# Kernel tuning notes

Measured on AMD Instinct MI355X. Metric: run time of the kernel, lower is better.

## Reference

```python
import jax, jax.numpy as jnp
import numpy as np

A_NUM = 9
C_NUM = 20


def generate_anchor(anc, grid):
    # anc: (A,2) w,h ; grid: (B,H,W,2) centers -> anchors (B,A,H,W,4)
    centers = grid[:, None]                      # (B,1,H,W,2)
    half = anc.reshape(1, -1, 1, 1, 2) * 0.5     # (1,A,1,1,2)
    return jnp.concatenate([centers - half, centers + half], axis=-1)


def iou_matrix(proposals, bboxes):
    # proposals: (B,A,H,W,4) -> (B,K,4); bboxes: (B,N,5)
    B = proposals.shape[0]
    p = proposals.reshape(B, -1, 4)[:, :, None, :]   # (B,K,1,4)
    bb = bboxes[:, None, :, :]                       # (B,1,N,5)
    s_p = (p[..., 2] - p[..., 0]) * (p[..., 3] - p[..., 1])
    s_b = (bb[..., 2] - bb[..., 0]) * (bb[..., 3] - bb[..., 1])
    ix1 = jnp.maximum(p[..., 0], bb[..., 0])
    iy1 = jnp.maximum(p[..., 1], bb[..., 1])
    ix2 = jnp.minimum(p[..., 2], bb[..., 2])
    iy2 = jnp.minimum(p[..., 3], bb[..., 3])
    s_i = jnp.clip(ix2 - ix1, 0.0) * jnp.clip(iy2 - iy1, 0.0)
    s_u = s_p + s_b - s_i
    iou = jnp.clip(s_i / (s_u + 1e-8), 0.0)
    invalid = (s_u <= 0) | (s_p <= 0) | (s_b <= 0) | (bb[..., 0] < 0)
    return jnp.where(invalid, 0.0, iou)              # (B,K,N)


def extract_anchor_data(anchor_data, idx):
    # anchor_data: (B,A,D,H,W) -> flat (B*A*H*W, D) -> gather
    B, A, D, H, W = anchor_data.shape
    flat = jnp.transpose(anchor_data, (0, 1, 3, 4, 2)).reshape(-1, D)
    return flat[idx]


def extract_class_scores(all_scores, idx, num_anchors):
    # all_scores: (B,C,H,W) -> (B,A,H,W,C) flat -> gather
    B, C, H, W = all_scores.shape
    s = jnp.transpose(all_scores, (0, 2, 3, 1))[:, None]          # (B,1,H,W,C)
    s = jnp.broadcast_to(s, (B, num_anchors, H, W, C)).reshape(-1, C)
    return s[idx]


def setup_inputs() -> dict:
    key = jax.random.key(0)
    ks = jax.random.split(key, 8)
    B, Cin, H, W = 32, 1280, 28, 28
    N, M = 64, 4096
    hid, out_ch = 128, 5 * A_NUM + C_NUM
    features = jax.random.normal(ks[0], (B, Cin, H, W), dtype=jnp.float32)
    # grid of feature-cell centers (GenerateGrid-style)
    xs = jnp.arange(W, dtype=jnp.float32) + 0.5
    ys = jnp.arange(H, dtype=jnp.float32) + 0.5
    gx, gy = jnp.meshgrid(xs, ys, indexing='xy')
    grid = jnp.broadcast_to(jnp.stack([gx, gy], axis=-1), (B, H, W, 2))
    anc = jnp.array([[1.0, 1], [2, 2], [3, 3], [4, 4], [5, 5], [2, 3], [3, 2], [3, 5], [5, 3]], dtype=jnp.float32)
    tl = jax.random.uniform(ks[1], (B, N, 2), minval=0.0, maxval=20.0)
    wh = jax.random.uniform(ks[2], (B, N, 2), minval=1.0, maxval=8.0)
    cls = jax.random.randint(ks[3], (B, N, 1), 0, C_NUM).astype(jnp.float32)
    bb = jnp.concatenate([tl, tl + wh, cls], axis=-1)
    valid = jax.random.uniform(ks[4], (B, N, 1)) > 0.25
    bboxes = jnp.where(valid, bb, -1.0)
    K = B * A_NUM * H * W
    pos_anchor_idx = jax.random.randint(ks[5], (M,), 0, K, dtype=jnp.int64 if jax.config.jax_enable_x64 else jnp.int32)
    neg_anchor_idx = jax.random.randint(ks[6], (M,), 0, K, dtype=pos_anchor_idx.dtype)
    W1 = jax.random.normal(ks[7], (hid, Cin), dtype=jnp.float32) * 0.02
    b1 = jnp.zeros((hid,), dtype=jnp.float32)
    W2 = jax.random.normal(jax.random.fold_in(key, 99), (out_ch, hid), dtype=jnp.float32) * 0.02
    b2 = jnp.zeros((out_ch,), dtype=jnp.float32)
    return {"features": features, "grid": grid, "anc": anc, "bboxes": bboxes,
            "pos_anchor_idx": pos_anchor_idx, "neg_anchor_idx": neg_anchor_idx,
            "W1": W1, "b1": b1, "W2": W2, "b2": b2}


def reference(features, grid, anc, bboxes, pos_anchor_idx, neg_anchor_idx, W1, b1, W2, b2):
    B, Cin, H, W = features.shape
    A, C = A_NUM, C_NUM
    # anchors + broadcast IoU matrix
    anchors = generate_anchor(anc, grid)                 # (B,A,H,W,4)
    iou_mat = iou_matrix(anchors, bboxes)                # (B,A*H*W,N)
    # prediction head: 1x1 conv -> (dropout eval: identity) -> leaky_relu -> 1x1 conv
    h = jnp.einsum('bchw,oc->bohw', features, W1) + b1[None, :, None, None]
    h = jax.nn.leaky_relu(h, negative_slope=0.01)
    out = jnp.einsum('bchw,oc->bohw', h, W2) + b2[None, :, None, None]  # (B,5A+C,H,W)
    anchor_raw = out[:, :5 * A].reshape(B, A, 5, H, W)
    conf_sq = jax.nn.sigmoid(anchor_raw[:, :, 0:1])      # (B,A,1,H,W)
    off_raw = anchor_raw[:, :, 1:]                       # (B,A,4,H,W)
    off_sq = jnp.concatenate([jax.nn.sigmoid(off_raw[:, :, :2]) - 0.5, off_raw[:, :, 2:]], axis=2)
    class_raw = out[:, 5 * A:]                           # (B,C,H,W)
    # training path: irregular gathers
    class_scores = extract_class_scores(class_raw, pos_anchor_idx, A)   # (M,C)
    offsets = extract_anchor_data(off_sq, pos_anchor_idx)               # (M,4)
    conf_pos = extract_anchor_data(conf_sq, pos_anchor_idx)             # (M,1)
    conf_neg = extract_anchor_data(conf_sq, neg_anchor_idx)             # (M,1)
    conf_scores = jnp.concatenate([conf_pos, conf_neg], axis=0)         # (2M,1)
    return conf_scores, offsets, class_scores, iou_mat
```

## Files before the change

### kernel.cpp

```cpp
#include <hip/hip_runtime.h>
#include <cstdint>

#define A_NUM 9
#define C_NUM 20
#define B_SZ 32
#define HW 784
#define P_NUM (A_NUM*HW)
#define NBOX 64
#define CIN 1280
#define HID 128
#define M_IDX 4096
#define KSPLIT 4
#define KS_PER 10
#define ASTR 40
#define PSTR ((size_t)B_SZ * HW * HID)
#define IOU_PB 64

#define CONF_OFF 0
#define OFFS_OFF (2*M_IDX)
#define CLS_OFF  (OFFS_OFF + 4*M_IDX)
#define IOU_OFF  (CLS_OFF + C_NUM*M_IDX)

typedef short bf16x8 __attribute__((ext_vector_type(8)));
typedef float f32x4  __attribute__((ext_vector_type(4)));

__device__ __forceinline__ unsigned pack_bf16(float lo, float hi) {
  unsigned a = __builtin_bit_cast(unsigned, lo);
  unsigned b = __builtin_bit_cast(unsigned, hi);
  return ((a + 0x8000u) >> 16) | ((b + 0x8000u) & 0xffff0000u);
}

__global__ __launch_bounds__(256) void prep_w1(const float* __restrict__ W1,
                                               uint4* __restrict__ W1f) {
  int id = blockIdx.x * 256 + threadIdx.x;
  int lane = id & 63;
  int ntile = (id >> 6) & 7;
  int ks = id >> 9;
  int lo = lane & 15, quad = lane >> 4;
  int n = ntile * 16 + lo;
  int k0 = ks * 32 + quad * 8;
  const float* src = W1 + n * CIN + k0;
  float4 x = *(const float4*)src;
  float4 y = *(const float4*)(src + 4);
  uint4 p;
  p.x = pack_bf16(x.x, x.y);
  p.y = pack_bf16(x.z, x.w);
  p.z = pack_bf16(y.x, y.y);
  p.w = pack_bf16(y.z, y.w);
  W1f[id] = p;
}

__global__ __launch_bounds__(256) void gemm1_mfma(
    const float* __restrict__ F, const unsigned short* __restrict__ W1f,
    float* __restrict__ Part) {
  __shared__ unsigned short Asm[2][64 * ASTR];

  const int b = blockIdx.y;
  const int z = blockIdx.z;
  const int m0 = blockIdx.x * 64;
  const int t = threadIdx.x;
  const int wave = t >> 6, lane = t & 63;
  const int quad = lane >> 4, lo = lane & 15;
  const int ksbase = z * KS_PER;

  const int sm = t & 63;
  const int kh = t >> 6;
  const int gm = m0 + sm;
  const bool mval = gm < HW;
  const float* Fb = F + (size_t)b * CIN * HW + (mval ? gm : 0);

  f32x4 acc[4][2];
#pragma unroll
  for (int i = 0; i < 4; i++)
#pragma unroll
    for (int j = 0; j < 2; j++) acc[i][j] = (f32x4){0.f, 0.f, 0.f, 0.f};

  float va[8];
  uint4 vb[2][2];

  auto loadA = [&](int kk) {
    const int k0 = (ksbase + kk) * 32 + kh * 8;
#pragma unroll
    for (int i = 0; i < 8; i++) va[i] = Fb[(size_t)(k0 + i) * HW];
  };
  auto loadB = [&](int kk, uint4* dst) {
    const unsigned short* g =
        W1f + (size_t)(((ksbase + kk) * 8 + wave * 2) * 64 + lane) * 8;
    dst[0] = *(const uint4*)g;
    dst[1] = *(const uint4*)(g + 512);
  };
  auto stageA = [&](int buf) {
    uint4 p;
    if (mval) {
      p.x = pack_bf16(va[0], va[1]);
      p.y = pack_bf16(va[2], va[3]);
      p.z = pack_bf16(va[4], va[5]);
      p.w = pack_bf16(va[6], va[7]);
    } else {
      p = (uint4){0, 0, 0, 0};
    }
    *(uint4*)&Asm[buf][sm * ASTR + kh * 8] = p;
  };
  auto compute = [&](int buf, uint4* bv) {
    const unsigned short* Ab = &Asm[buf][lo * ASTR + quad * 8];
    bf16x8 af[4];
#pragma unroll
    for (int i = 0; i < 4; i++) af[i] = *(const bf16x8*)(Ab + i * 16 * ASTR);
    bf16x8 b0 = __builtin_bit_cast(bf16x8, bv[0]);
    bf16x8 b1 = __builtin_bit_cast(bf16x8, bv[1]);
#pragma unroll
    for (int i = 0; i < 4; i++) {
      acc[i][0] = __builtin_amdgcn_mfma_f32_16x16x32_bf16(af[i], b0, acc[i][0], 0, 0, 0);
      acc[i][1] = __builtin_amdgcn_mfma_f32_16x16x32_bf16(af[i], b1, acc[i][1], 0, 0, 0);
    }
  };

  loadA(0);
  loadB(0, vb[0]);
  stageA(0);
  __syncthreads();
  for (int kk = 0; kk < KS_PER; kk++) {
    const int cur = kk & 1;
    if (kk + 1 < KS_PER) {
      loadA(kk + 1);
      loadB(kk + 1, vb[cur ^ 1]);
    }
    compute(cur, vb[cur]);
    if (kk + 1 < KS_PER) stageA(cur ^ 1);
    __syncthreads();
  }

  float* Pz = Part + ((size_t)(z * B_SZ + b) * HW) * HID;
#pragma unroll
  for (int i = 0; i < 4; i++) {
    const int mbase = m0 + i * 16 + quad * 4;
#pragma unroll
    for (int j = 0; j < 2; j++) {
      const int n = wave * 32 + j * 16 + lo;
#pragma unroll
      for (int r = 0; r < 4; r++) {
        const int mm = mbase + r;
        if (mm < HW) Pz[(size_t)mm * HID + n] = acc[i][j][r];
      }
    }
  }
}

__global__ __launch_bounds__(256) void iou_kernel(
    const float* __restrict__ grid, const float* __restrict__ anc,
    const float* __restrict__ bboxes, float* __restrict__ out) {
  __shared__ float sb[NBOX * 5];
  __shared__ float4 sp4[IOU_PB];
  const int b = blockIdx.y;
  const int p0 = blockIdx.x * IOU_PB;
  const int t = threadIdx.x;
  for (int i = t; i < NBOX * 5; i += 256) sb[i] = bboxes[b * NBOX * 5 + i];
  if (t < IOU_PB) {
    int p = p0 + t;
    float x1 = 0.f, y1 = 0.f, x2 = 0.f, y2 = 0.f;
    if (p < P_NUM) {
      int a = p / HW, hw = p - a * HW;
      float2 c = ((const float2*)grid)[b * HW + hw];
      float hx = anc[a * 2 + 0] * 0.5f, hy = anc[a * 2 + 1] * 0.5f;
      x1 = c.x - hx; y1 = c.y - hy; x2 = c.x + hx; y2 = c.y + hy;
    }
    sp4[t] = make_float4(x1, y1, x2, y2);
  }
  __syncthreads();
  const int nl = (t & 15) * 4;
  const int pi = t >> 4;
#pragma unroll
  for (int ip = 0; ip < 4; ip++) {
    const int pl = pi + 16 * ip;
    const int p = p0 + pl;
    const float4 pb = sp4[pl];
    const float spA = (pb.z - pb.x) * (pb.w - pb.y);
    float4 res;
#pragma unroll
    for (int jn = 0; jn < 4; jn++) {
      const int n = nl + jn;
      float bx1 = sb[n * 5 + 0], by1 = sb[n * 5 + 1];
      float bx2 = sb[n * 5 + 2], by2 = sb[n * 5 + 3];
      float s_b = (bx2 - bx1) * (by2 - by1);
      float ix1 = fmaxf(pb.x, bx1), iy1 = fmaxf(pb.y, by1);
      float ix2 = fminf(pb.z, bx2), iy2 = fminf(pb.w, by2);
      float si = fmaxf(ix2 - ix1, 0.f) * fmaxf(iy2 - iy1, 0.f);
      float su = spA + s_b - si;
      float iou = fmaxf(si / (su + 1e-8f), 0.f);
      bool invalid = (su <= 0.f) | (spA <= 0.f) | (s_b <= 0.f) | (bx1 < 0.f);
      float v = invalid ? 0.f : iou;
      if (jn == 0) res.x = v; else if (jn == 1) res.y = v;
      else if (jn == 2) res.z = v; else res.w = v;
    }
    if (p < P_NUM)
      *(float4*)&out[((size_t)(b * P_NUM + p)) * 64 + nl] = res;
  }
}

__global__ __launch_bounds__(256) void gather_kernel(
    const int* __restrict__ pos_idx, const int* __restrict__ neg_idx,
    const float* __restrict__ Part, const float* __restrict__ b1,
    const float* __restrict__ W2, const float* __restrict__ b2,
    float* __restrict__ out) {
  __shared__ float sh[4][HID];
  const int sub = threadIdx.x >> 6;
  const int l = threadIdx.x & 63;
  const int blk = blockIdx.x * 4 + sub;
  const bool pos = blk < M_IDX;
  const int idx = pos ? pos_idx[blk] : neg_idx[blk - M_IDX];
  const int b = idx / P_NUM;
  const int r = idx - b * P_NUM;
  const int a = r / HW;
  const int hw = r - a * HW;
  const float2* row = (const float2*)(Part + ((size_t)(b * HW + hw)) * HID) + l;
  float2 s0 = row[0];
  float2 s1 = row[PSTR / 2];
  float2 s2 = row[2 * (PSTR / 2)];
  float2 s3 = row[3 * (PSTR / 2)];
  float v0 = s0.x + s1.x + s2.x + s3.x + b1[2 * l];
  float v1 = s0.y + s1.y + s2.y + s3.y + b1[2 * l + 1];
  v0 = v0 > 0.f ? v0 : 0.01f * v0;
  v1 = v1 > 0.f ? v1 : 0.01f * v1;
  sh[sub][2 * l] = v0; sh[sub][2 * l + 1] = v1;
  __syncthreads();
  if (pos) {
    if (l < 25) {
      int o = (l < 5) ? (a * 5 + l) : (5 * A_NUM + (l - 5));
      const float* w = W2 + o * HID;
      float dot = b2[o];
#pragma unroll 8
      for (int k = 0; k < HID; k++) dot = fmaf(w[k], sh[sub][k], dot);
      if (l == 0) {
        out[CONF_OFF + blk] = 1.f / (1.f + expf(-dot));
      } else if (l < 3) {
        out[OFFS_OFF + blk * 4 + (l - 1)] = 1.f / (1.f + expf(-dot)) - 0.5f;
      } else if (l < 5) {
        out[OFFS_OFF + blk * 4 + (l - 1)] = dot;
      } else {
        out[CLS_OFF + blk * C_NUM + (l - 5)] = dot;
      }
    }
  } else {
    int o = a * 5;
    const float* w = W2 + o * HID;
    float part = fmaf(w[2 * l], v0, w[2 * l + 1] * v1);
#pragma unroll
    for (int off = 32; off > 0; off >>= 1) part += __shfl_down(part, off);
    if (l == 0) out[CONF_OFF + blk] = 1.f / (1.f + expf(-(b2[o] + part)));
  }
}

extern "C" void kernel_launch(void* const* d_in, const int* in_sizes, int n_in,
                              void* d_out, int out_size, void* d_ws, size_t ws_size,
                              hipStream_t stream) {
  const float* features = (const float*)d_in[0];
  const float* grid     = (const float*)d_in[1];
  const float* anc      = (const float*)d_in[2];
  const float* bboxes   = (const float*)d_in[3];
  const int*   pos_idx  = (const int*)d_in[4];
  const int*   neg_idx  = (const int*)d_in[5];
  const float* W1       = (const float*)d_in[6];
  const float* b1       = (const float*)d_in[7];
  const float* W2       = (const float*)d_in[8];
  const float* b2       = (const float*)d_in[9];
  float* out = (float*)d_out;

  uint4* W1f = (uint4*)d_ws;
  float* Part = (float*)((char*)d_ws + 327680);

  hipLaunchKernelGGL(prep_w1, dim3(80), dim3(256), 0, stream, W1, W1f);
  hipLaunchKernelGGL(gemm1_mfma, dim3(13, B_SZ, KSPLIT), dim3(256), 0, stream,
                     features, (const unsigned short*)W1f, Part);
  hipLaunchKernelGGL(iou_kernel, dim3((P_NUM + IOU_PB - 1) / IOU_PB, B_SZ),
                     dim3(256), 0, stream, grid, anc, bboxes, out + IOU_OFF);
  hipLaunchKernelGGL(gather_kernel, dim3(2 * M_IDX / 4), dim3(256),
                     0, stream, pos_idx, neg_idx, Part, b1, W2, b2, out);
}
```

Measured before the change: 262.5 us.

## Pre-transpose features to bf16 HW-major layout and halve GEMM K-split

```diff
diff --git a/kernel.cpp b/kernel.cpp
--- a/kernel.cpp
+++ b/kernel.cpp
@@ -10,11 +10,12 @@
 #define CIN 1280
 #define HID 128
 #define M_IDX 4096
-#define KSPLIT 4
-#define KS_PER 10
+#define KSPLIT 2
 #define ASTR 40
 #define PSTR ((size_t)B_SZ * HW * HID)
 #define IOU_PB 64
+#define TP_HW 196
+#define TP_S 197
 
 #define CONF_OFF 0
 #define OFFS_OFF (2*M_IDX)
@@ -28,6 +29,43 @@
   unsigned a = __builtin_bit_cast(unsigned, lo);
   unsigned b = __builtin_bit_cast(unsigned, hi);
   return ((a + 0x8000u) >> 16) | ((b + 0x8000u) & 0xffff0000u);
+}
+
+__global__ __launch_bounds__(256) void transpose_pack(
+    const float* __restrict__ F, unsigned* __restrict__ Ft) {
+  __shared__ unsigned T2[32 * TP_S];
+  const int b = blockIdx.z;
+  const int cc = blockIdx.y;
+  const int hc = blockIdx.x;
+  const int t = threadIdx.x;
+  const int c0 = cc * 64, hw0 = hc * TP_HW;
+  const float* Fb = F + ((size_t)b * CIN + c0) * HW + hw0;
+  for (int i = 0; i < 7; i++) {
+    int slot = t + 256 * i;
+    if (slot < 1568) {
+      int rp = slot / 49, ch = slot - rp * 49;
+      const float* s0 = Fb + (size_t)(2 * rp) * HW + ch * 4;
+      float4 lo4 = *(const float4*)s0;
+      float4 hi4 = *(const float4*)(s0 + HW);
+      unsigned* d = &T2[rp * TP_S + ch * 4];
+      d[0] = pack_bf16(lo4.x, hi4.x);
+      d[1] = pack_bf16(lo4.y, hi4.y);
+      d[2] = pack_bf16(lo4.z, hi4.z);
+      d[3] = pack_bf16(lo4.w, hi4.w);
+    }
+  }
+  __syncthreads();
+  unsigned* Fo = Ft + ((size_t)b * HW + hw0) * (CIN / 2) + c0 / 2;
+  for (int i = 0; i < 13; i++) {
+    int id = t + 256 * i;
+    if (id < 3136) {
+      int hw = id >> 4, ch = id & 15;
+      uint2 v;
+      v.x = T2[(2 * ch) * TP_S + hw];
+      v.y = T2[(2 * ch + 1) * TP_S + hw];
+      *(uint2*)&Fo[(size_t)hw * (CIN / 2) + ch * 2] = v;
+    }
+  }
 }
 
 __global__ __launch_bounds__(256) void prep_w1(const float* __restrict__ W1,
@@ -51,23 +89,19 @@
 }
 
 __global__ __launch_bounds__(256) void gemm1_mfma(
-    const float* __restrict__ F, const unsigned short* __restrict__ W1f,
+    const unsigned short* __restrict__ Ft, const unsigned short* __restrict__ W1f,
     float* __restrict__ Part) {
   __shared__ unsigned short Asm[2][64 * ASTR];
 
-  const int b = blockIdx.y;
-  const int z = blockIdx.z;
+  const int b = blockIdx.y, z = blockIdx.z;
   const int m0 = blockIdx.x * 64;
   const int t = threadIdx.x;
   const int wave = t >> 6, lane = t & 63;
   const int quad = lane >> 4, lo = lane & 15;
-  const int ksbase = z * KS_PER;
-
-  const int sm = t & 63;
-  const int kh = t >> 6;
+  const int sm = t >> 2, kc = t & 3;
   const int gm = m0 + sm;
-  const bool mval = gm < HW;
-  const float* Fb = F + (size_t)b * CIN * HW + (mval ? gm : 0);
+  const unsigned short* Fr =
+      Ft + ((size_t)b * HW + (gm < HW ? gm : 0)) * CIN + z * 640;
 
   f32x4 acc[4][2];
 #pragma unroll
@@ -75,31 +109,18 @@
 #pragma unroll
     for (int j = 0; j < 2; j++) acc[i][j] = (f32x4){0.f, 0.f, 0.f, 0.f};
 
-  float va[8];
+  uint4 va;
   uint4 vb[2][2];
 
-  auto loadA = [&](int kk) {
-    const int k0 = (ksbase + kk) * 32 + kh * 8;
-#pragma unroll
-    for (int i = 0; i < 8; i++) va[i] = Fb[(size_t)(k0 + i) * HW];
-  };
+  auto loadA = [&](int kk) { va = *(const uint4*)(Fr + kk * 32 + kc * 8); };
   auto loadB = [&](int kk, uint4* dst) {
     const unsigned short* g =
-        W1f + (size_t)(((ksbase + kk) * 8 + wave * 2) * 64 + lane) * 8;
+        W1f + (size_t)((((z * 20 + kk) * 8) + wave * 2) * 64 + lane) * 8;
     dst[0] = *(const uint4*)g;
     dst[1] = *(const uint4*)(g + 512);
   };
   auto stageA = [&](int buf) {
-    uint4 p;
-    if (mval) {
-      p.x = pack_bf16(va[0], va[1]);
-      p.y = pack_bf16(va[2], va[3]);
-      p.z = pack_bf16(va[4], va[5]);
-      p.w = pack_bf16(va[6], va[7]);
-    } else {
-      p = (uint4){0, 0, 0, 0};
-    }
-    *(uint4*)&Asm[buf][sm * ASTR + kh * 8] = p;
+    *(uint4*)&Asm[buf][sm * ASTR + kc * 8] = va;
   };
   auto compute = [&](int buf, uint4* bv) {
     const unsigned short* Ab = &Asm[buf][lo * ASTR + quad * 8];
@@ -119,14 +140,14 @@
   loadB(0, vb[0]);
   stageA(0);
   __syncthreads();
-  for (int kk = 0; kk < KS_PER; kk++) {
+  for (int kk = 0; kk < 20; kk++) {
     const int cur = kk & 1;
-    if (kk + 1 < KS_PER) {
+    if (kk + 1 < 20) {
       loadA(kk + 1);
       loadB(kk + 1, vb[cur ^ 1]);
     }
     compute(cur, vb[cur]);
-    if (kk + 1 < KS_PER) stageA(cur ^ 1);
+    if (kk + 1 < 20) stageA(cur ^ 1);
     __syncthreads();
   }
 
@@ -215,10 +236,8 @@
   const float2* row = (const float2*)(Part + ((size_t)(b * HW + hw)) * HID) + l;
   float2 s0 = row[0];
   float2 s1 = row[PSTR / 2];
-  float2 s2 = row[2 * (PSTR / 2)];
-  float2 s3 = row[3 * (PSTR / 2)];
-  float v0 = s0.x + s1.x + s2.x + s3.x + b1[2 * l];
-  float v1 = s0.y + s1.y + s2.y + s3.y + b1[2 * l + 1];
+  float v0 = s0.x + s1.x + b1[2 * l];
+  float v1 = s0.y + s1.y + b1[2 * l + 1];
   v0 = v0 > 0.f ? v0 : 0.01f * v0;
   v1 = v1 > 0.f ? v1 : 0.01f * v1;
   sh[sub][2 * l] = v0; sh[sub][2 * l + 1] = v1;
@@ -266,11 +285,14 @@
   float* out = (float*)d_out;
 
   uint4* W1f = (uint4*)d_ws;
-  float* Part = (float*)((char*)d_ws + 327680);
-
+  unsigned* Ft = (unsigned*)((char*)d_ws + 327680);
+  float* Part = (float*)((char*)d_ws + 327680 + 64225280);
+
+  hipLaunchKernelGGL(transpose_pack, dim3(4, 20, B_SZ), dim3(256), 0, stream,
+                     features, Ft);
   hipLaunchKernelGGL(prep_w1, dim3(80), dim3(256), 0, stream, W1, W1f);
   hipLaunchKernelGGL(gemm1_mfma, dim3(13, B_SZ, KSPLIT), dim3(256), 0, stream,
-                     features, (const unsigned short*)W1f, Part);
+                     (const unsigned short*)Ft, (const unsigned short*)W1f, Part);
   hipLaunchKernelGGL(iou_kernel, dim3((P_NUM + IOU_PB - 1) / IOU_PB, B_SZ),
                      dim3(256), 0, stream, grid, anc, bboxes, out + IOU_OFF);
   hipLaunchKernelGGL(gather_kernel, dim3(2 * M_IDX / 4), dim3(256),
```

Result: slower. 276.3 us (+5.3%).
